# Kernel optimization log

Measured on AMD Instinct MI355X. Metric: run time of the kernel, lower is better.

Reference implementation:

```python
import jax, jax.numpy as jnp
import numpy as np

N_NODES = 50000


def _gcn_layer(x, src, dst, W, b, n_nodes):
    # x: [N, Cin] -> linear -> [N, Cout]
    h = x @ W.T + b
    # degree over destination (col) index, including self loops
    deg = jax.ops.segment_sum(jnp.ones(src.shape[0], dtype=x.dtype), dst,
                              num_segments=n_nodes)
    dinv = jnp.where(deg > 0, deg ** -0.5, jnp.zeros((), x.dtype))
    norm = dinv[src] * dinv[dst]                      # [E]
    msg = h[src] * norm[:, None]                      # gather + scale
    return jax.ops.segment_sum(msg, dst, num_segments=n_nodes)  # scatter-add


def setup_inputs() -> dict:
    key = jax.random.key(0)
    k1, k2, k3, k4, k5, k6 = jax.random.split(key, 6)
    num_features = 128
    hidden_dim = 128
    n_edges = 1_600_000
    x = jax.random.normal(k1, (N_NODES, num_features), dtype=jnp.float32)
    edge_index = jax.random.randint(k2, (2, n_edges), 0, N_NODES, dtype=jnp.int64)
    bound1 = 1.0 / np.sqrt(num_features)
    W1 = jax.random.uniform(k3, (hidden_dim, num_features), jnp.float32, -bound1, bound1)
    b1 = jax.random.uniform(k4, (hidden_dim,), jnp.float32, -bound1, bound1)
    bound2 = 1.0 / np.sqrt(hidden_dim)
    W2 = jax.random.uniform(k5, (hidden_dim, hidden_dim), jnp.float32, -bound2, bound2)
    b2 = jax.random.uniform(k6, (hidden_dim,), jnp.float32, -bound2, bound2)
    return {"x": x, "edge_index": edge_index, "W1": W1, "b1": b1, "W2": W2, "b2": b2}


def reference(x, edge_index, W1, b1, W2, b2):
    n_nodes = x.shape[0]
    # add_self_loops: append (i, i) for every node
    loops = jnp.arange(n_nodes, dtype=edge_index.dtype)
    src = jnp.concatenate([edge_index[0], loops])
    dst = jnp.concatenate([edge_index[1], loops])
    h = _gcn_layer(x, src, dst, W1, b1, n_nodes)
    h = jax.nn.relu(h)
    # dropout is identity in eval mode (deterministic reference)
    out = _gcn_layer(h, src, dst, W2, b2, n_nodes)
    return out
```

## Files before the change

### kernel.cpp

```cpp
#include <hip/hip_runtime.h>


static constexpr int F = 128;
static constexpr int NR = 128;
static constexpr int CH = 4096;
static constexpr int RMAX = 512;

typedef __attribute__((ext_vector_type(8))) short bf16x8;
typedef __attribute__((ext_vector_type(4))) float f32x4;

__device__ __forceinline__ unsigned f2b(float x) {
  unsigned u = __float_as_uint(x);
  return (u + 0x7fffu + ((u >> 16) & 1u)) >> 16;
}
__device__ __forceinline__ float b_lo(unsigned u) {
  return __uint_as_float(u << 16);
}
__device__ __forceinline__ float b_hi(unsigned u) {
  return __uint_as_float(u & 0xffff0000u);
}

__global__ void k_zero_i32(int* __restrict__ p, int n) {
  int i = blockIdx.x * blockDim.x + threadIdx.x;
  if (i < n) p[i] = 0;
}

__global__ __launch_bounds__(256) void k_hist(const int* __restrict__ dst,
                                              int E, int R,
                                              int* __restrict__ rtot) {
  __shared__ int h[RMAX];
  for (int i = threadIdx.x; i < R; i += 256) h[i] = 0;
  __syncthreads();
  const int e0 = blockIdx.x * CH;
  const int e1 = min(e0 + CH, E);
  for (int i = e0 + threadIdx.x; i < e1; i += 256)
    atomicAdd(&h[dst[i] >> 7], 1);
  __syncthreads();
  for (int i = threadIdx.x; i < R; i += 256)
    if (h[i]) atomicAdd(&rtot[i], h[i]);
}

__global__ __launch_bounds__(512) void k_scanR(const int* __restrict__ rtot,
                                               int R, int E,
                                               int* __restrict__ rbase,
                                               int* __restrict__ gcur) {
  __shared__ int s[512];
  const int t = threadIdx.x;
  const int v = (t < R) ? rtot[t] : 0;
  s[t] = v;
  __syncthreads();
#pragma unroll
  for (int off = 1; off < 512; off <<= 1) {
    int a = (t >= off) ? s[t - off] : 0;
    __syncthreads();
    s[t] += a;
    __syncthreads();
  }
  if (t < R) {
    const int b = s[t] - v;
    rbase[t] = b;
    gcur[t] = b;
  }
  if (t == 0) rbase[R] = E;
}

__global__ __launch_bounds__(256) void k_part(const int* __restrict__ src,
                                              const int* __restrict__ dst,
                                              int E, int R,
                                              int* __restrict__ gcur,
                                              unsigned* __restrict__ rsorted) {
  __shared__ int h[RMAX];
  __shared__ int cur[RMAX];
  for (int i = threadIdx.x; i < R; i += 256) h[i] = 0;
  __syncthreads();
  const int e0 = blockIdx.x * CH;
  const int e1 = min(e0 + CH, E);
  for (int i = e0 + threadIdx.x; i < e1; i += 256)
    atomicAdd(&h[dst[i] >> 7], 1);
  __syncthreads();
  for (int i = threadIdx.x; i < R; i += 256)
    cur[i] = h[i] ? atomicAdd(&gcur[i], h[i]) : 0;
  __syncthreads();
  for (int i = e0 + threadIdx.x; i < e1; i += 256) {
    const int d = dst[i];
    const int s = src[i];
    const int pos = atomicAdd(&cur[d >> 7], 1);
    rsorted[pos] = ((unsigned)(d & (NR - 1)) << 16) | (unsigned)s;
  }
}

__global__ __launch_bounds__(256) void k_fillR(
    const unsigned* __restrict__ rsorted, const int* __restrict__ rbase,
    int N, int E, int* __restrict__ rowptr, float* __restrict__ dinv,
    int* __restrict__ csr) {
  __shared__ int cnt[NR];
  __shared__ int sc[NR];
  __shared__ int cur[NR];
  const int r = blockIdx.x;
  const int tid = threadIdx.x;
  const int b = rbase[r];
  const int e = rbase[r + 1];
  if (tid < NR) cnt[tid] = 0;
  __syncthreads();
  for (int i = b + tid; i < e; i += 256)
    atomicAdd(&cnt[rsorted[i] >> 16], 1);
  __syncthreads();
  if (tid < NR) sc[tid] = cnt[tid];
  __syncthreads();
#pragma unroll
  for (int off = 1; off < NR; off <<= 1) {
    int a = (tid < NR && tid >= off) ? sc[tid - off] : 0;
    __syncthreads();
    if (tid < NR) sc[tid] += a;
    __syncthreads();
  }
  if (tid < NR) {
    const int excl = sc[tid] - cnt[tid];
    cur[tid] = excl;
    const int node = r * NR + tid;
    if (node < N) {
      rowptr[node] = b + excl;
      dinv[node] = rsqrtf((float)(cnt[tid] + 1));
    }
  }
  if (r == 0 && tid == 0) rowptr[N] = E;
  __syncthreads();
  for (int i = b + tid; i < e; i += 256) {
    const unsigned v = rsorted[i];
    const int pos = b + atomicAdd(&cur[v >> 16], 1);
    csr[pos] = (int)(v & 0xFFFFu);
  }
}

__global__ __launch_bounds__(256) void k_splitW(const float* __restrict__ W,
                                                unsigned short* __restrict__ hi,
                                                unsigned short* __restrict__ lo) {
  const int i = blockIdx.x * 256 + threadIdx.x;
  const int j = i & 7;
  const int lane = (i >> 3) & 63;
  const int f = (i >> 9) & 7;
  const int t = i >> 12;
  const int col = f * 16 + (lane & 15);
  const int k = t * 32 + ((j & 4) << 2) + 4 * (lane >> 4) + (j & 3);
  const float x = W[col * F + k];
  const unsigned h = f2b(x);
  hi[i] = (unsigned short)h;
  lo[i] = (unsigned short)f2b(x - __uint_as_float(h << 16));
}

__global__ __launch_bounds__(256) void k_gemm_mfma(
    const float* __restrict__ A, const unsigned short* __restrict__ Whi,
    const unsigned short* __restrict__ Wlo, const float* __restrict__ bias,
    const float* __restrict__ dinv, unsigned short* __restrict__ hout, int n) {
  const int wid = threadIdx.x >> 6;
  const int lane = threadIdx.x & 63;
  const int r = lane & 15;
  const int g = lane >> 4;
  const int m0 = blockIdx.x * 64 + wid * 16;
  const int arow = m0 + r;

  f32x4 acc[8];
#pragma unroll
  for (int f = 0; f < 8; ++f) acc[f] = (f32x4){0.f, 0.f, 0.f, 0.f};

#pragma unroll
  for (int t = 0; t < 4; ++t) {
    bf16x8 bhi[8], blo[8];
#pragma unroll
    for (int f = 0; f < 8; ++f) {
      const size_t base = (((size_t)t * 8 + f) * 64 + lane) * 8;
      bhi[f] = *(const bf16x8*)(Whi + base);
      blo[f] = *(const bf16x8*)(Wlo + base);
    }
    const int kt = t * 32;
    float4 a0 = make_float4(0.f, 0.f, 0.f, 0.f);
    float4 a1 = make_float4(0.f, 0.f, 0.f, 0.f);
    if (arow < n) {
      a0 = *(const float4*)(A + (size_t)arow * F + kt + 4 * g);
      a1 = *(const float4*)(A + (size_t)arow * F + kt + 16 + 4 * g);
    }
    bf16x8 ahi, alo;
    {
      unsigned h;
      h = f2b(a0.x); ahi[0] = (short)h; alo[0] = (short)f2b(a0.x - __uint_as_float(h << 16));
      h = f2b(a0.y); ahi[1] = (short)h; alo[1] = (short)f2b(a0.y - __uint_as_float(h << 16));
      h = f2b(a0.z); ahi[2] = (short)h; alo[2] = (short)f2b(a0.z - __uint_as_float(h << 16));
      h = f2b(a0.w); ahi[3] = (short)h; alo[3] = (short)f2b(a0.w - __uint_as_float(h << 16));
      h = f2b(a1.x); ahi[4] = (short)h; alo[4] = (short)f2b(a1.x - __uint_as_float(h << 16));
      h = f2b(a1.y); ahi[5] = (short)h; alo[5] = (short)f2b(a1.y - __uint_as_float(h << 16));
      h = f2b(a1.z); ahi[6] = (short)h; alo[6] = (short)f2b(a1.z - __uint_as_float(h << 16));
      h = f2b(a1.w); ahi[7] = (short)h; alo[7] = (short)f2b(a1.w - __uint_as_float(h << 16));
    }
#pragma unroll
    for (int f = 0; f < 8; ++f) {
      acc[f] = __builtin_amdgcn_mfma_f32_16x16x32_bf16(ahi, bhi[f], acc[f], 0, 0, 0);
      acc[f] = __builtin_amdgcn_mfma_f32_16x16x32_bf16(ahi, blo[f], acc[f], 0, 0, 0);
      acc[f] = __builtin_amdgcn_mfma_f32_16x16x32_bf16(alo, bhi[f], acc[f], 0, 0, 0);
    }
  }

  int orow[4];
  float dv[4];
#pragma unroll
  for (int j = 0; j < 4; ++j) {
    orow[j] = m0 + 4 * g + j;
    dv[j] = (orow[j] < n) ? dinv[orow[j]] : 0.f;
  }
#pragma unroll
  for (int f = 0; f < 8; ++f) {
    const int col = f * 16 + r;
    const float bv = bias[col];
#pragma unroll
    for (int j = 0; j < 4; ++j) {
      if (orow[j] < n)
        hout[(size_t)orow[j] * F + col] = (unsigned short)f2b((acc[f][j] + bv) * dv[j]);
    }
  }
}

template <bool RELU>
__global__ __launch_bounds__(256) void k_pull(
    const int* __restrict__ rowptr, const int* __restrict__ csr,
    const uint2* __restrict__ h, const float* __restrict__ dinv,
    float* __restrict__ out, int n) {
  const int wid = (blockIdx.x * blockDim.x + threadIdx.x) >> 6;
  if (wid >= n) return;
  const int lane = threadIdx.x & 63;
  const int half = lane >> 5;
  const int l32 = lane & 31;
  const int beg = rowptr[wid];
  const int end = rowptr[wid + 1];

  float4 acc = make_float4(0.f, 0.f, 0.f, 0.f);
  if (half == 0) {
    const uint2 u = h[(size_t)wid * 32 + l32];
    acc.x = b_lo(u.x); acc.y = b_hi(u.x);
    acc.z = b_lo(u.y); acc.w = b_hi(u.y);
  }

  int k = beg + half;
  for (; k + 6 < end; k += 8) {
    const int s0 = csr[k];
    const int s1 = csr[k + 2];
    const int s2 = csr[k + 4];
    const int s3 = csr[k + 6];
    const uint2 u0 = h[(size_t)s0 * 32 + l32];
    const uint2 u1 = h[(size_t)s1 * 32 + l32];
    const uint2 u2 = h[(size_t)s2 * 32 + l32];
    const uint2 u3 = h[(size_t)s3 * 32 + l32];
    acc.x += b_lo(u0.x) + b_lo(u1.x) + b_lo(u2.x) + b_lo(u3.x);
    acc.y += b_hi(u0.x) + b_hi(u1.x) + b_hi(u2.x) + b_hi(u3.x);
    acc.z += b_lo(u0.y) + b_lo(u1.y) + b_lo(u2.y) + b_lo(u3.y);
    acc.w += b_hi(u0.y) + b_hi(u1.y) + b_hi(u2.y) + b_hi(u3.y);
  }
  for (; k < end; k += 2) {
    const uint2 u = h[(size_t)csr[k] * 32 + l32];
    acc.x += b_lo(u.x);
    acc.y += b_hi(u.x);
    acc.z += b_lo(u.y);
    acc.w += b_hi(u.y);
  }

  acc.x += __shfl_xor(acc.x, 32, 64);
  acc.y += __shfl_xor(acc.y, 32, 64);
  acc.z += __shfl_xor(acc.z, 32, 64);
  acc.w += __shfl_xor(acc.w, 32, 64);

  if (half == 0) {
    const float dv = dinv[wid];
    float4 r;
    r.x = acc.x * dv;
    r.y = acc.y * dv;
    r.z = acc.z * dv;
    r.w = acc.w * dv;
    if (RELU) {
      r.x = fmaxf(r.x, 0.f);
      r.y = fmaxf(r.y, 0.f);
      r.z = fmaxf(r.z, 0.f);
      r.w = fmaxf(r.w, 0.f);
    }
    ((float4*)out)[(size_t)wid * 32 + l32] = r;
  }
}

extern "C" void kernel_launch(void* const* d_in, const int* in_sizes, int n_in,
                              void* d_out, int out_size, void* d_ws, size_t ws_size,
                              hipStream_t stream) {
  const float* x  = (const float*)d_in[0];
  const int*   ei = (const int*)d_in[1];
  const float* W1 = (const float*)d_in[2];
  const float* b1 = (const float*)d_in[3];
  const float* W2 = (const float*)d_in[4];
  const float* b2 = (const float*)d_in[5];

  const int N = in_sizes[0] / F;
  const int E = in_sizes[1] / 2;
  const int* src = ei;
  const int* dst = ei + E;
  const int R = (N + NR - 1) / NR;
  const int C = (E + CH - 1) / CH;

  char* ws = (char*)d_ws;
  int*            rtot    = (int*)(ws);
  int*            rbase   = (int*)(ws + (4u << 10));
  int*            gcur    = (int*)(ws + (8u << 10));
  float*          dinv    = (float*)(ws + (16u << 10));
  int*            rowptr  = (int*)(ws + (256u << 10));
  unsigned short* Whi1    = (unsigned short*)(ws + (480u << 10));
  unsigned short* Wlo1    = (unsigned short*)(ws + (512u << 10));
  unsigned short* Whi2    = (unsigned short*)(ws + (544u << 10));
  unsigned short* Wlo2    = (unsigned short*)(ws + (576u << 10));
  unsigned*       rsorted = (unsigned*)(ws + (1u << 20));
  int*            csr     = (int*)(ws + (8u << 20));
  unsigned short* hbuf    = (unsigned short*)(ws + (16u << 20));
  float*          out     = (float*)d_out;

  const int B = 256;
  const int gemmBlocks = (N + 63) / 64;
  const int pullBlocks = (N * 64 + B - 1) / B;

  k_zero_i32<<<(R + 255) / 256, B, 0, stream>>>(rtot, R);
  k_hist<<<C, B, 0, stream>>>(dst, E, R, rtot);
  k_scanR<<<1, 512, 0, stream>>>(rtot, R, E, rbase, gcur);
  k_part<<<C, B, 0, stream>>>(src, dst, E, R, gcur, rsorted);
  k_fillR<<<R, B, 0, stream>>>(rsorted, rbase, N, E, rowptr, dinv, csr);
  k_splitW<<<64, B, 0, stream>>>(W1, Whi1, Wlo1);
  k_splitW<<<64, B, 0, stream>>>(W2, Whi2, Wlo2);

  k_gemm_mfma<<<gemmBlocks, B, 0, stream>>>(x, Whi1, Wlo1, b1, dinv, hbuf, N);
  k_pull<true><<<pullBlocks, B, 0, stream>>>(rowptr, csr, (const uint2*)hbuf, dinv, out, N);

  k_gemm_mfma<<<gemmBlocks, B, 0, stream>>>(out, Whi2, Wlo2, b2, dinv, hbuf, N);
  k_pull<false><<<pullBlocks, B, 0, stream>>>(rowptr, csr, (const uint2*)hbuf, dinv, out, N);
}
```

Baseline: 214.9 us.

## Split pull aggregation into feature quarters with 16-bit CSR indices

The pull kernel now has each block handle four nodes for one quarter of the feature columns (32 features). Each 16-lane slot gathers one 4-byte word per neighbour, and block indices are interleaved so the four quarters of the same node group run close together in time. CSR column indices are stored as 16-bit values, halving index traffic, and the index loads and output stores use nontemporal hints. The aim is a smaller working set per pass and less index bandwidth, at the cost of reading the index list four times and issuing narrower gathers. The 16-bit indices only hold node ids below 65536.

```diff
diff --git a/kernel.cpp b/kernel.cpp
--- a/kernel.cpp
+++ b/kernel.cpp
@@ -92,7 +92,7 @@
 __global__ __launch_bounds__(256) void k_fillR(
     const unsigned* __restrict__ rsorted, const int* __restrict__ rbase,
     int N, int E, int* __restrict__ rowptr, float* __restrict__ dinv,
-    int* __restrict__ csr) {
+    unsigned short* __restrict__ csr) {
   __shared__ int cnt[NR];
   __shared__ int sc[NR];
   __shared__ int cur[NR];
@@ -128,7 +128,7 @@
   for (int i = b + tid; i < e; i += 256) {
     const unsigned v = rsorted[i];
     const int pos = b + atomicAdd(&cur[v >> 16], 1);
-    csr[pos] = (int)(v & 0xFFFFu);
+    csr[pos] = (unsigned short)(v & 0xFFFFu);
   }
 }
 
@@ -220,66 +220,65 @@
 
 template <bool RELU>
 __global__ __launch_bounds__(256) void k_pull(
-    const int* __restrict__ rowptr, const int* __restrict__ csr,
-    const uint2* __restrict__ h, const float* __restrict__ dinv,
+    const int* __restrict__ rowptr, const unsigned short* __restrict__ csr,
+    const unsigned* __restrict__ hb, const float* __restrict__ dinv,
     float* __restrict__ out, int n) {
-  const int wid = (blockIdx.x * blockDim.x + threadIdx.x) >> 6;
-  if (wid >= n) return;
+  const int b = blockIdx.x;
+  const int q = (b & 7) >> 1;
+  const int ng = ((b >> 3) << 1) | (b & 1);
+  const int node = ng * 4 + (threadIdx.x >> 6);
+  if (node >= n) return;
   const int lane = threadIdx.x & 63;
-  const int half = lane >> 5;
-  const int l32 = lane & 31;
-  const int beg = rowptr[wid];
-  const int end = rowptr[wid + 1];
-
-  float4 acc = make_float4(0.f, 0.f, 0.f, 0.f);
-  if (half == 0) {
-    const uint2 u = h[(size_t)wid * 32 + l32];
-    acc.x = b_lo(u.x); acc.y = b_hi(u.x);
-    acc.z = b_lo(u.y); acc.w = b_hi(u.y);
-  }
-
-  int k = beg + half;
-  for (; k + 6 < end; k += 8) {
-    const int s0 = csr[k];
-    const int s1 = csr[k + 2];
-    const int s2 = csr[k + 4];
-    const int s3 = csr[k + 6];
-    const uint2 u0 = h[(size_t)s0 * 32 + l32];
-    const uint2 u1 = h[(size_t)s1 * 32 + l32];
-    const uint2 u2 = h[(size_t)s2 * 32 + l32];
-    const uint2 u3 = h[(size_t)s3 * 32 + l32];
-    acc.x += b_lo(u0.x) + b_lo(u1.x) + b_lo(u2.x) + b_lo(u3.x);
-    acc.y += b_hi(u0.x) + b_hi(u1.x) + b_hi(u2.x) + b_hi(u3.x);
-    acc.z += b_lo(u0.y) + b_lo(u1.y) + b_lo(u2.y) + b_lo(u3.y);
-    acc.w += b_hi(u0.y) + b_hi(u1.y) + b_hi(u2.y) + b_hi(u3.y);
-  }
-  for (; k < end; k += 2) {
-    const uint2 u = h[(size_t)csr[k] * 32 + l32];
-    acc.x += b_lo(u.x);
-    acc.y += b_hi(u.x);
-    acc.z += b_lo(u.y);
-    acc.w += b_hi(u.y);
-  }
-
+  const int slot = lane >> 4;
+  const int fi = lane & 15;
+  const unsigned* __restrict__ hq = hb + q * 16;
+
+  const int beg = rowptr[node];
+  const int end = rowptr[node + 1];
+
+  float2 acc = make_float2(0.f, 0.f);
+  if (slot == 0) {
+    const unsigned u = hq[(size_t)node * 64 + fi];
+    acc.x = b_lo(u);
+    acc.y = b_hi(u);
+  }
+
+  int k = beg + slot;
+  for (; k + 12 < end; k += 16) {
+    const int s0 = __builtin_nontemporal_load(csr + k);
+    const int s1 = __builtin_nontemporal_load(csr + k + 4);
+    const int s2 = __builtin_nontemporal_load(csr + k + 8);
+    const int s3 = __builtin_nontemporal_load(csr + k + 12);
+    const unsigned u0 = hq[(size_t)s0 * 64 + fi];
+    const unsigned u1 = hq[(size_t)s1 * 64 + fi];
+    const unsigned u2 = hq[(size_t)s2 * 64 + fi];
+    const unsigned u3 = hq[(size_t)s3 * 64 + fi];
+    acc.x += b_lo(u0) + b_lo(u1) + b_lo(u2) + b_lo(u3);
+    acc.y += b_hi(u0) + b_hi(u1) + b_hi(u2) + b_hi(u3);
+  }
+  for (; k < end; k += 4) {
+    const int s = __builtin_nontemporal_load(csr + k);
+    const unsigned u = hq[(size_t)s * 64 + fi];
+    acc.x += b_lo(u);
+    acc.y += b_hi(u);
+  }
+
+  acc.x += __shfl_xor(acc.x, 16, 64);
+  acc.y += __shfl_xor(acc.y, 16, 64);
   acc.x += __shfl_xor(acc.x, 32, 64);
   acc.y += __shfl_xor(acc.y, 32, 64);
-  acc.z += __shfl_xor(acc.z, 32, 64);
-  acc.w += __shfl_xor(acc.w, 32, 64);
-
-  if (half == 0) {
-    const float dv = dinv[wid];
-    float4 r;
-    r.x = acc.x * dv;
-    r.y = acc.y * dv;
-    r.z = acc.z * dv;
-    r.w = acc.w * dv;
+
+  if (slot == 0) {
+    const float dv = dinv[node];
+    float rx = acc.x * dv;
+    float ry = acc.y * dv;
     if (RELU) {
-      r.x = fmaxf(r.x, 0.f);
-      r.y = fmaxf(r.y, 0.f);
-      r.z = fmaxf(r.z, 0.f);
-      r.w = fmaxf(r.w, 0.f);
-    }
-    ((float4*)out)[(size_t)wid * 32 + l32] = r;
+      rx = fmaxf(rx, 0.f);
+      ry = fmaxf(ry, 0.f);
+    }
+    float* po = out + (size_t)node * F + q * 32 + fi * 2;
+    __builtin_nontemporal_store(rx, po);
+    __builtin_nontemporal_store(ry, po + 1);
   }
 }
 
@@ -311,13 +310,14 @@
   unsigned short* Whi2    = (unsigned short*)(ws + (544u << 10));
   unsigned short* Wlo2    = (unsigned short*)(ws + (576u << 10));
   unsigned*       rsorted = (unsigned*)(ws + (1u << 20));
-  int*            csr     = (int*)(ws + (8u << 20));
-  unsigned short* hbuf    = (unsigned short*)(ws + (16u << 20));
+  unsigned short* csr     = (unsigned short*)(ws + (8u << 20));
+  unsigned*       hbuf    = (unsigned*)(ws + (16u << 20));
   float*          out     = (float*)d_out;
 
   const int B = 256;
   const int gemmBlocks = (N + 63) / 64;
-  const int pullBlocks = (N * 64 + B - 1) / B;
+  const int ng2 = (((N + 3) / 4) + 1) & ~1;
+  const int pullBlocks = 4 * ng2;
 
   k_zero_i32<<<(R + 255) / 256, B, 0, stream>>>(rtot, R);
   k_hist<<<C, B, 0, stream>>>(dst, E, R, rtot);
@@ -327,9 +327,11 @@
   k_splitW<<<64, B, 0, stream>>>(W1, Whi1, Wlo1);
   k_splitW<<<64, B, 0, stream>>>(W2, Whi2, Wlo2);
 
-  k_gemm_mfma<<<gemmBlocks, B, 0, stream>>>(x, Whi1, Wlo1, b1, dinv, hbuf, N);
-  k_pull<true><<<pullBlocks, B, 0, stream>>>(rowptr, csr, (const uint2*)hbuf, dinv, out, N);
-
-  k_gemm_mfma<<<gemmBlocks, B, 0, stream>>>(out, Whi2, Wlo2, b2, dinv, hbuf, N);
-  k_pull<false><<<pullBlocks, B, 0, stream>>>(rowptr, csr, (const uint2*)hbuf, dinv, out, N);
-}
+  k_gemm_mfma<<<gemmBlocks, B, 0, stream>>>(x, Whi1, Wlo1, b1, dinv,
+                                            (unsigned short*)hbuf, N);
+  k_pull<true><<<pullBlocks, B, 0, stream>>>(rowptr, csr, hbuf, dinv, out, N);
+
+  k_gemm_mfma<<<gemmBlocks, B, 0, stream>>>(out, Whi2, Wlo2, b2, dinv,
+                                            (unsigned short*)hbuf, N);
+  k_pull<false><<<pullBlocks, B, 0, stream>>>(rowptr, csr, hbuf, dinv, out, N);
+}
```

Result: slower. 380.4 us (+77.0%).
